# Kernel tuning notes

Measured on AMD Instinct MI355X. Metric: run time of the kernel, lower is better.

The kernel has to match this reference:

```python
import jax, jax.numpy as jnp
import numpy as np

B, T, D, H = 4, 1024, 1024, 16
HD = D // H
EPS = 1e-5


def setup_inputs() -> dict:
    key = jax.random.key(0)
    ks = jax.random.split(key, 8)
    input_tensor = jax.random.normal(ks[0], (B, T, D), dtype=jnp.float32)
    # contiguous valid prefixes (realistic padding mask); True = valid
    lengths = jax.random.randint(ks[1], (B,), T // 2, T + 1)
    sequence_mask = jnp.arange(T)[None, :] < lengths[:, None]
    # online attention mask: causal (True = position allowed)
    attn_mask = jnp.tril(jnp.ones((T, T), dtype=bool))
    scale = 1.0 / np.sqrt(D)
    in_proj_w = jax.random.normal(ks[2], (3 * D, D), dtype=jnp.float32) * scale
    in_proj_b = jnp.zeros((3 * D,), dtype=jnp.float32)
    out_w = jax.random.normal(ks[3], (D, D), dtype=jnp.float32) * scale
    out_b = jnp.zeros((D,), dtype=jnp.float32)
    ln_gamma = jnp.ones((D,), dtype=jnp.float32)
    ln_beta = jnp.zeros((D,), dtype=jnp.float32)
    return {
        "input_tensor": input_tensor,
        "ln_gamma": ln_gamma,
        "ln_beta": ln_beta,
        "in_proj_w": in_proj_w,
        "in_proj_b": in_proj_b,
        "out_w": out_w,
        "out_b": out_b,
        "sequence_mask": sequence_mask,
        "attn_mask": attn_mask,
    }


def reference(input_tensor, ln_gamma, ln_beta, in_proj_w, in_proj_b, out_w, out_b,
              sequence_mask, attn_mask):
    # LayerNorm over last dim
    mu = jnp.mean(input_tensor, axis=-1, keepdims=True)
    var = jnp.mean(jnp.square(input_tensor - mu), axis=-1, keepdims=True)
    x = (input_tensor - mu) * jax.lax.rsqrt(var + EPS) * ln_gamma + ln_beta

    # shared QKV projection (torch MHA packed in_proj)
    qkv = x @ in_proj_w.T + in_proj_b  # [B,T,3D]
    q, k, v = jnp.split(qkv, 3, axis=-1)
    q = q.reshape(B, T, H, HD) * (1.0 / np.sqrt(HD))
    k = k.reshape(B, T, H, HD)
    v = v.reshape(B, T, H, HD)

    scores = jnp.einsum("bqhd,bkhd->bhqk", q, k)  # [B,H,T,T], shared

    keypad = sequence_mask[:, None, None, :]          # True = valid key
    online_ok = keypad & attn_mask[None, None, :, :]  # padding + attn mask
    neg_inf = jnp.float32(-jnp.inf)

    def attend(ok_mask):
        p = jax.nn.softmax(jnp.where(ok_mask, scores, neg_inf), axis=-1)
        o = jnp.einsum("bhqk,bkhd->bqhd", p, v).reshape(B, T, D)
        return o @ out_w.T + out_b

    out_online = attend(online_ok)   # key_padding + attn_mask
    out_offline = attend(keypad)     # key_padding only (full context)
    # training path: cat on dim 0 then view(2, B, T, D)
    return jnp.stack((out_online, out_offline), axis=0)
```

## Files before the change

kernel.cpp:

```cpp
#include <hip/hip_runtime.h>

#define B_ 4
#define T_ 1024
#define D_ 1024
#define H_ 16
#define HD_ 64

typedef unsigned short u16;
typedef __bf16 bf16x8 __attribute__((ext_vector_type(8)));
typedef float f32x4 __attribute__((ext_vector_type(4)));
typedef unsigned short u16x4 __attribute__((ext_vector_type(4)));

__device__ inline u16 f2b(float f) {
    union { float f; unsigned u; } v; v.f = f;
    unsigned r = v.u + 0x7fffu + ((v.u >> 16) & 1u);
    return (u16)(r >> 16);
}

__device__ inline f32x4 mfma16(bf16x8 a, bf16x8 b, f32x4 c) {
    return __builtin_amdgcn_mfma_f32_16x16x32_bf16(a, b, c, 0, 0, 0);
}

__global__ __launch_bounds__(256) void len_kernel(const unsigned char* __restrict__ m,
                                                  int* __restrict__ lens) {
    const int t = threadIdx.x;
    const int b = blockIdx.x;
    const int esz4 = (m[1] == 0);
    int c = 0;
    for (int i = t; i < T_; i += 256) {
        bool v = esz4 ? (((const int*)m)[b * T_ + i] != 0) : (m[b * T_ + i] != 0);
        c += v ? 1 : 0;
    }
#pragma unroll
    for (int off = 1; off < 64; off <<= 1) c += __shfl_xor(c, off);
    __shared__ int red[4];
    if ((t & 63) == 0) red[t >> 6] = c;
    __syncthreads();
    if (t == 0) lens[b] = red[0] + red[1] + red[2] + red[3];
}

__global__ __launch_bounds__(256) void cvt_bf16(const float* __restrict__ in,
                                                u16* __restrict__ out, int n4) {
    int i = blockIdx.x * 256 + threadIdx.x;
    int stride = gridDim.x * 256;
    for (; i < n4; i += stride) {
        float4 v = ((const float4*)in)[i];
        u16x4 o = { f2b(v.x), f2b(v.y), f2b(v.z), f2b(v.w) };
        ((u16x4*)out)[i] = o;
    }
}

__global__ __launch_bounds__(256) void ln_kernel(const float* __restrict__ x,
                                                 const float* __restrict__ g,
                                                 const float* __restrict__ be,
                                                 u16* __restrict__ y) {
    __shared__ float red[8];
    const int row = blockIdx.x;
    const int tid = threadIdx.x;
    const float* xr = x + (size_t)row * D_;
    float4 v = ((const float4*)xr)[tid];
    float s  = v.x + v.y + v.z + v.w;
    float ss = v.x*v.x + v.y*v.y + v.z*v.z + v.w*v.w;
#pragma unroll
    for (int off = 1; off < 64; off <<= 1) {
        s  += __shfl_xor(s, off);
        ss += __shfl_xor(ss, off);
    }
    const int w = tid >> 6;
    if ((tid & 63) == 0) { red[w*2] = s; red[w*2+1] = ss; }
    __syncthreads();
    s  = red[0] + red[2] + red[4] + red[6];
    ss = red[1] + red[3] + red[5] + red[7];
    const float mu = s * (1.f/1024.f);
    const float rs = rsqrtf(ss*(1.f/1024.f) - mu*mu + 1e-5f);
    float4 gv = ((const float4*)g)[tid];
    float4 bv = ((const float4*)be)[tid];
    u16x4 o = { f2b((v.x-mu)*rs*gv.x + bv.x),
                f2b((v.y-mu)*rs*gv.y + bv.y),
                f2b((v.z-mu)*rs*gv.z + bv.z),
                f2b((v.w-mu)*rs*gv.w + bv.w) };
    ((u16x4*)(y + (size_t)row * D_))[tid] = o;
}

template <int EPI>
__global__ __launch_bounds__(256) void gemm_bt(
    const u16* __restrict__ A, const u16* __restrict__ Bw,
    const float* __restrict__ bias, float* __restrict__ Cf,
    u16* __restrict__ Qb, u16* __restrict__ Kb, u16* __restrict__ Vt,
    int M, int N, int K) {
    __shared__ u16 As[2][128 * 64];
    __shared__ u16 Bs[2][128 * 64];
    const int tid = threadIdx.x;
    const int w = tid >> 6, l = tid & 63;
    const int l15 = l & 15, lg = l >> 4;
    const int m0 = blockIdx.y * 128, n0 = blockIdx.x * 128;
    const int wr = w >> 1, wc = w & 1;
    const int srow = l >> 3;
    const int scg  = (l & 7) ^ srow;
    const int swa  = l15 & 7;

    f32x4 acc[4][4];
#pragma unroll
    for (int m = 0; m < 4; m++)
#pragma unroll
        for (int n = 0; n < 4; n++) acc[m][n] = (f32x4){0.f, 0.f, 0.f, 0.f};

    const int KS = K >> 6;

    auto stage = [&](int buf, int ks) {
        const int k0 = ks * 64;
#pragma unroll
        for (int it = 0; it < 4; ++it) {
            const int c = it * 4 + w;
            const int row = c * 8 + srow;
            const u16* ga = A  + (size_t)(m0 + row) * K + (k0 + scg * 8);
            const u16* gb = Bw + (size_t)(n0 + row) * K + (k0 + scg * 8);
            __builtin_amdgcn_global_load_lds(
                (const __attribute__((address_space(1))) unsigned int*)ga,
                (__attribute__((address_space(3))) unsigned int*)(&As[buf][c * 512]), 16, 0, 0);
            __builtin_amdgcn_global_load_lds(
                (const __attribute__((address_space(1))) unsigned int*)gb,
                (__attribute__((address_space(3))) unsigned int*)(&Bs[buf][c * 512]), 16, 0, 0);
        }
    };

    stage(0, 0);

    int buf = 0;
    for (int ks = 0; ks < KS; ++ks) {
        if (ks + 1 < KS) {
            stage(buf ^ 1, ks + 1);
            asm volatile("s_waitcnt vmcnt(8)" ::: "memory");
        } else {
            asm volatile("s_waitcnt vmcnt(0)" ::: "memory");
        }
        __builtin_amdgcn_sched_barrier(0);
        __builtin_amdgcn_s_barrier();
        __builtin_amdgcn_sched_barrier(0);
#pragma unroll
        for (int h = 0; h < 2; ++h) {
            bf16x8 af[4], bfr[4];
#pragma unroll
            for (int m = 0; m < 4; m++)
                af[m] = *(const bf16x8*)&As[buf][(wr*64 + m*16 + l15) * 64 + ((h*4 + lg) ^ swa) * 8];
#pragma unroll
            for (int n = 0; n < 4; n++)
                bfr[n] = *(const bf16x8*)&Bs[buf][(wc*64 + n*16 + l15) * 64 + ((h*4 + lg) ^ swa) * 8];
#pragma unroll
            for (int m = 0; m < 4; m++)
#pragma unroll
                for (int n = 0; n < 4; n++)
                    acc[m][n] = mfma16(af[m], bfr[n], acc[m][n]);
        }
        __builtin_amdgcn_sched_barrier(0);
        __builtin_amdgcn_s_barrier();
        __builtin_amdgcn_sched_barrier(0);
        buf ^= 1;
    }

#pragma unroll
    for (int m = 0; m < 4; m++) {
#pragma unroll
        for (int n = 0; n < 4; n++) {
            const int col = n0 + wc*64 + n*16 + l15;
            const float bv = bias[col];
            if constexpr (EPI == 0) {
#pragma unroll
                for (int r = 0; r < 4; r++) {
                    const int row = m0 + wr*64 + m*16 + lg*4 + r;
                    Cf[(size_t)row * N + col] = acc[m][n][r] + bv;
                }
            } else {
                const int which = col >> 10;
                const int d = col & 1023;
                const int h = d >> 6, hd = d & 63;
#pragma unroll
                for (int r = 0; r < 4; r++) {
                    const int row = m0 + wr*64 + m*16 + lg*4 + r;
                    const int bb = row >> 10, t = row & 1023;
                    const float v = acc[m][n][r] + bv;
                    const size_t bh = (size_t)bb * H_ + h;
                    if (which == 0)      Qb[(bh * T_ + t) * HD_ + hd] = f2b(v * 0.125f);
                    else if (which == 1) Kb[(bh * T_ + t) * HD_ + hd] = f2b(v);
                    else                 Vt[(bh * HD_ + hd) * T_ + t] = f2b(v);
                }
            }
        }
    }
}

__global__ __launch_bounds__(256) void attn_kernel(
    const u16* __restrict__ Qb, const u16* __restrict__ Kb,
    const u16* __restrict__ Vt, const int* __restrict__ lens,
    u16* __restrict__ Ob) {
    __shared__ u16 Ks[2][64 * 64];
    __shared__ u16 Vs[2][64 * 64];
    __shared__ char Pl[4][2048];
    const int qt  = blockIdx.x;
    const int bh  = blockIdx.y;
    const int b = bh >> 4, h = bh & 15;
    const int tid = threadIdx.x, w = tid >> 6, l = tid & 63;
    const int l15 = l & 15, lg = l >> 4;
    const int len = lens[b];

    const u16* Qh = Qb + (size_t)bh * (T_ * HD_);
    const u16* Kh = Kb + (size_t)bh * (T_ * HD_);
    const u16* Vh = Vt + (size_t)bh * (HD_ * T_);

    const int q0 = qt * 64 + w * 16;
    const int qrow = q0 + l15;

    const bf16x8 qf0 = *(const bf16x8*)(Qh + (size_t)qrow * HD_ + lg * 8);
    const bf16x8 qf1 = *(const bf16x8*)(Qh + (size_t)qrow * HD_ + 32 + lg * 8);

    f32x4 acc0[4], acc1[4];
#pragma unroll
    for (int n = 0; n < 4; n++) {
        acc0[n] = (f32x4){0.f, 0.f, 0.f, 0.f};
        acc1[n] = (f32x4){0.f, 0.f, 0.f, 0.f};
    }
    float l0p = 0.f, l1p = 0.f;

    const int ntk = (len + 63) >> 6;

    char* Pw = &Pl[w][0];
    const int swz = (l15 & 7) << 4;
    const int rsw = l15 & 7;

    const int srow = l >> 3;
    const int scg  = (l & 7) ^ srow;

    const float C1 = 1.44269504f, C0 = -28.8539008f;

    auto stage = [&](int buf, int kt) {
        const int k0 = kt * 64;
#pragma unroll
        for (int c = 0; c < 2; ++c) {
            const int row = (w*2 + c)*8 + srow;
            const u16* gk = Kh + (size_t)(k0 + row) * HD_ + scg*8;
            const u16* gv = Vh + (size_t)row * T_ + k0 + scg*8;
            __builtin_amdgcn_global_load_lds(
                (const __attribute__((address_space(1))) unsigned int*)gk,
                (__attribute__((address_space(3))) unsigned int*)(&Ks[buf][(w*2+c)*512]), 16, 0, 0);
            __builtin_amdgcn_global_load_lds(
                (const __attribute__((address_space(1))) unsigned int*)gv,
                (__attribute__((address_space(3))) unsigned int*)(&Vs[buf][(w*2+c)*512]), 16, 0, 0);
        }
    };

    stage(0, 0);
    __syncthreads();

    int buf = 0;
    for (int kt = 0; kt < ntk; ++kt) {
        if (kt + 1 < ntk) stage(buf ^ 1, kt + 1);
        const int k0 = kt * 64;
        const u16* Kt = &Ks[buf][0];
        const u16* Vl = &Vs[buf][0];

        f32x4 s[4];
#pragma unroll
        for (int n = 0; n < 4; n++) {
            const u16* kr = Kt + (n*16 + l15) * 64;
            bf16x8 kf0 = *(const bf16x8*)&kr[((0 + lg) ^ rsw) * 8];
            bf16x8 kf1 = *(const bf16x8*)&kr[((4 + lg) ^ rsw) * 8];
            f32x4 z = (f32x4){0.f, 0.f, 0.f, 0.f};
            z = mfma16(kf0, qf0, z);
            z = mfma16(kf1, qf1, z);
            s[n] = z;
        }
        bf16x8 vf[4][2];
#pragma unroll
        for (int n = 0; n < 4; n++) {
            const u16* vr = Vl + (n*16 + l15) * 64;
            vf[n][0] = *(const bf16x8*)&vr[((0 + lg) ^ rsw) * 8];
            vf[n][1] = *(const bf16x8*)&vr[((4 + lg) ^ rsw) * 8];
        }
        float pn = 0.f;
#pragma unroll
        for (int n = 0; n < 4; n++) {
            const int kb = k0 + n*16 + lg*4;
#pragma unroll
            for (int r = 0; r < 4; r++) {
                const float e = (kb + r < len) ? exp2f(s[n][r]*C1 + C0) : 0.f;
                s[n][r] = e;
                pn += e;
            }
        }
        const bool diag = (kt == qt);
        if (diag) {
            l0p = l1p;
#pragma unroll
            for (int n = 0; n < 4; n++) acc0[n] = acc1[n];
        }
        l1p += pn;
#pragma unroll
        for (int n = 0; n < 4; n++) {
            u16x4 pk = { f2b(s[n][0]), f2b(s[n][1]), f2b(s[n][2]), f2b(s[n][3]) };
            *(u16x4*)(Pw + ((l15*128 + n*32 + lg*8) ^ swz)) = pk;
        }
#pragma unroll
        for (int kk = 0; kk < 2; ++kk) {
            bf16x8 pa = *(const bf16x8*)(Pw + ((l15*128 + kk*64 + lg*16) ^ swz));
#pragma unroll
            for (int n = 0; n < 4; n++)
                acc1[n] = mfma16(vf[n][kk], pa, acc1[n]);
        }
        if (diag) {
            float pn0 = 0.f;
#pragma unroll
            for (int n = 0; n < 4; n++) {
                const int kb = k0 + n*16 + lg*4;
#pragma unroll
                for (int r = 0; r < 4; r++) {
                    const float e = (kb + r <= qrow) ? s[n][r] : 0.f;
                    s[n][r] = e;
                    pn0 += e;
                }
            }
            l0p += pn0;
#pragma unroll
            for (int n = 0; n < 4; n++) {
                u16x4 pk = { f2b(s[n][0]), f2b(s[n][1]), f2b(s[n][2]), f2b(s[n][3]) };
                *(u16x4*)(Pw + ((l15*128 + n*32 + lg*8) ^ swz)) = pk;
            }
#pragma unroll
            for (int kk = 0; kk < 2; ++kk) {
                bf16x8 pa = *(const bf16x8*)(Pw + ((l15*128 + kk*64 + lg*16) ^ swz));
#pragma unroll
                for (int n = 0; n < 4; n++)
                    acc0[n] = mfma16(vf[n][kk], pa, acc0[n]);
            }
        }
        __syncthreads();
        buf ^= 1;
    }

    if (qt >= ntk) {
        l0p = l1p;
#pragma unroll
        for (int n = 0; n < 4; n++) acc0[n] = acc1[n];
    }

    float l0 = l0p + __shfl_xor(l0p, 16);
    l0 += __shfl_xor(l0, 32);
    float l1 = l1p + __shfl_xor(l1p, 16);
    l1 += __shfl_xor(l1, 32);

    const float inv0 = 1.f / l0;
    const float inv1 = 1.f / l1;
    u16* O0 = Ob + ((size_t)b * T_ + qrow) * D_ + h * HD_;
    u16* O1 = O0 + (size_t)B_ * T_ * D_;
#pragma unroll
    for (int n = 0; n < 4; n++) {
        u16x4 o0 = { f2b(acc0[n][0] * inv0), f2b(acc0[n][1] * inv0),
                     f2b(acc0[n][2] * inv0), f2b(acc0[n][3] * inv0) };
        u16x4 o1 = { f2b(acc1[n][0] * inv1), f2b(acc1[n][1] * inv1),
                     f2b(acc1[n][2] * inv1), f2b(acc1[n][3] * inv1) };
        *(u16x4*)(O0 + n*16 + lg*4) = o0;
        *(u16x4*)(O1 + n*16 + lg*4) = o1;
    }
}

extern "C" void kernel_launch(void* const* d_in, const int* in_sizes, int n_in,
                              void* d_out, int out_size, void* d_ws, size_t ws_size,
                              hipStream_t stream) {
    const float* x_in   = (const float*)d_in[0];
    const float* gamma  = (const float*)d_in[1];
    const float* beta   = (const float*)d_in[2];
    const float* wqkv_f = (const float*)d_in[3];
    const float* bqkv   = (const float*)d_in[4];
    const float* wout_f = (const float*)d_in[5];
    const float* bout   = (const float*)d_in[6];
    const unsigned char* smask = (const unsigned char*)d_in[7];
    float* out = (float*)d_out;

    char* ws = (char*)d_ws;
    u16* xb   = (u16*)(ws);
    u16* wqkv = (u16*)(ws + ((size_t)8  << 20));
    u16* wo   = (u16*)(ws + ((size_t)14 << 20));
    u16* Qb   = (u16*)(ws + ((size_t)16 << 20));
    u16* Kb   = (u16*)(ws + ((size_t)24 << 20));
    u16* Vt   = (u16*)(ws + ((size_t)32 << 20));
    u16* Ob   = (u16*)(ws + ((size_t)40 << 20));
    int* lens = (int*)(ws + ((size_t)56 << 20));

    len_kernel<<<dim3(B_), dim3(256), 0, stream>>>(smask, lens);
    cvt_bf16<<<dim3(1024), dim3(256), 0, stream>>>(wqkv_f, wqkv, (3 * D_ * D_) / 4);
    cvt_bf16<<<dim3(512),  dim3(256), 0, stream>>>(wout_f, wo, (D_ * D_) / 4);
    ln_kernel<<<dim3(B_ * T_), dim3(256), 0, stream>>>(x_in, gamma, beta, xb);
    gemm_bt<1><<<dim3(24, 32), dim3(256), 0, stream>>>(
        xb, wqkv, bqkv, nullptr, Qb, Kb, Vt, B_ * T_, 3 * D_, D_);
    attn_kernel<<<dim3(T_ / 64, B_ * H_), dim3(256), 0, stream>>>(Qb, Kb, Vt, lens, Ob);
    gemm_bt<0><<<dim3(8, 64), dim3(256), 0, stream>>>(
        Ob, wo, bout, out, nullptr, nullptr, nullptr, 2 * B_ * T_, D_, D_);
}
```

Baseline: 146.4 us.

## Enlarge GEMM tiles to 256x256 with 8 waves and XCD-aware block swizzle

Both projection GEMMs now use 256x256 output tiles computed by 512-thread blocks, with each wave owning a 128x64 sub-tile, and launch on a 1D grid. Block indices are remapped so that consecutive tiles land on the same XCD, which should improve L2 reuse. The larger tiles cut global and LDS traffic per FLOP. In exchange, LDS use per block rises to 128KB and accumulator register pressure doubles, which limits occupancy, and the grids shrink to 192 and 128 blocks on a GPU with 256 CUs, so some CUs sit idle.

New measurement: 166.5 us. 1.14x slower.

```diff
diff --git a/kernel.cpp b/kernel.cpp
--- a/kernel.cpp
+++ b/kernel.cpp
@@ -83,25 +83,32 @@
 }
 
 template <int EPI>
-__global__ __launch_bounds__(256) void gemm_bt(
+__global__ __launch_bounds__(512) void gemm_bt(
     const u16* __restrict__ A, const u16* __restrict__ Bw,
     const float* __restrict__ bias, float* __restrict__ Cf,
     u16* __restrict__ Qb, u16* __restrict__ Kb, u16* __restrict__ Vt,
-    int M, int N, int K) {
-    __shared__ u16 As[2][128 * 64];
-    __shared__ u16 Bs[2][128 * 64];
+    int M, int N, int K, int MB) {
+    __shared__ u16 As[2][256 * 64];
+    __shared__ u16 Bs[2][256 * 64];
     const int tid = threadIdx.x;
     const int w = tid >> 6, l = tid & 63;
     const int l15 = l & 15, lg = l >> 4;
-    const int m0 = blockIdx.y * 128, n0 = blockIdx.x * 128;
-    const int wr = w >> 1, wc = w & 1;
+    const int wr = w >> 2, wc = w & 3;
+
+    const int nwg = gridDim.x;
+    const int q8 = nwg >> 3, r8 = nwg & 7;
+    const int xcd = blockIdx.x & 7, pos = blockIdx.x >> 3;
+    const int swz = (xcd < r8 ? xcd * (q8 + 1) : r8 * (q8 + 1) + (xcd - r8) * q8) + pos;
+    const int m0 = (swz % MB) * 256;
+    const int n0 = (swz / MB) * 256;
+
     const int srow = l >> 3;
     const int scg  = (l & 7) ^ srow;
     const int swa  = l15 & 7;
 
-    f32x4 acc[4][4];
-#pragma unroll
-    for (int m = 0; m < 4; m++)
+    f32x4 acc[8][4];
+#pragma unroll
+    for (int m = 0; m < 8; m++)
 #pragma unroll
         for (int n = 0; n < 4; n++) acc[m][n] = (f32x4){0.f, 0.f, 0.f, 0.f};
 
@@ -111,7 +118,7 @@
         const int k0 = ks * 64;
 #pragma unroll
         for (int it = 0; it < 4; ++it) {
-            const int c = it * 4 + w;
+            const int c = w * 4 + it;
             const int row = c * 8 + srow;
             const u16* ga = A  + (size_t)(m0 + row) * K + (k0 + scg * 8);
             const u16* gb = Bw + (size_t)(n0 + row) * K + (k0 + scg * 8);
@@ -139,18 +146,17 @@
         __builtin_amdgcn_sched_barrier(0);
 #pragma unroll
         for (int h = 0; h < 2; ++h) {
-            bf16x8 af[4], bfr[4];
-#pragma unroll
-            for (int m = 0; m < 4; m++)
-                af[m] = *(const bf16x8*)&As[buf][(wr*64 + m*16 + l15) * 64 + ((h*4 + lg) ^ swa) * 8];
+            bf16x8 bfr[4];
 #pragma unroll
             for (int n = 0; n < 4; n++)
                 bfr[n] = *(const bf16x8*)&Bs[buf][(wc*64 + n*16 + l15) * 64 + ((h*4 + lg) ^ swa) * 8];
 #pragma unroll
-            for (int m = 0; m < 4; m++)
+            for (int m = 0; m < 8; m++) {
+                bf16x8 af = *(const bf16x8*)&As[buf][(wr*128 + m*16 + l15) * 64 + ((h*4 + lg) ^ swa) * 8];
 #pragma unroll
                 for (int n = 0; n < 4; n++)
-                    acc[m][n] = mfma16(af[m], bfr[n], acc[m][n]);
+                    acc[m][n] = mfma16(af, bfr[n], acc[m][n]);
+            }
         }
         __builtin_amdgcn_sched_barrier(0);
         __builtin_amdgcn_s_barrier();
@@ -159,7 +165,7 @@
     }
 
 #pragma unroll
-    for (int m = 0; m < 4; m++) {
+    for (int m = 0; m < 8; m++) {
 #pragma unroll
         for (int n = 0; n < 4; n++) {
             const int col = n0 + wc*64 + n*16 + l15;
@@ -167,7 +173,7 @@
             if constexpr (EPI == 0) {
 #pragma unroll
                 for (int r = 0; r < 4; r++) {
-                    const int row = m0 + wr*64 + m*16 + lg*4 + r;
+                    const int row = m0 + wr*128 + m*16 + lg*4 + r;
                     Cf[(size_t)row * N + col] = acc[m][n][r] + bv;
                 }
             } else {
@@ -176,7 +182,7 @@
                 const int h = d >> 6, hd = d & 63;
 #pragma unroll
                 for (int r = 0; r < 4; r++) {
-                    const int row = m0 + wr*64 + m*16 + lg*4 + r;
+                    const int row = m0 + wr*128 + m*16 + lg*4 + r;
                     const int bb = row >> 10, t = row & 1023;
                     const float v = acc[m][n][r] + bv;
                     const size_t bh = (size_t)bb * H_ + h;
@@ -389,9 +395,9 @@
     cvt_bf16<<<dim3(1024), dim3(256), 0, stream>>>(wqkv_f, wqkv, (3 * D_ * D_) / 4);
     cvt_bf16<<<dim3(512),  dim3(256), 0, stream>>>(wout_f, wo, (D_ * D_) / 4);
     ln_kernel<<<dim3(B_ * T_), dim3(256), 0, stream>>>(x_in, gamma, beta, xb);
-    gemm_bt<1><<<dim3(24, 32), dim3(256), 0, stream>>>(
-        xb, wqkv, bqkv, nullptr, Qb, Kb, Vt, B_ * T_, 3 * D_, D_);
+    gemm_bt<1><<<dim3(192), dim3(512), 0, stream>>>(
+        xb, wqkv, bqkv, nullptr, Qb, Kb, Vt, B_ * T_, 3 * D_, D_, 16);
     attn_kernel<<<dim3(T_ / 64, B_ * H_), dim3(256), 0, stream>>>(Qb, Kb, Vt, lens, Ob);
-    gemm_bt<0><<<dim3(8, 64), dim3(256), 0, stream>>>(
-        Ob, wo, bout, out, nullptr, nullptr, nullptr, 2 * B_ * T_, D_, D_);
-}
+    gemm_bt<0><<<dim3(128), dim3(512), 0, stream>>>(
+        Ob, wo, bout, out, nullptr, nullptr, nullptr, 2 * B_ * T_, D_, D_, 32);
+}
```
